# Kernel optimization log

Measured on AMD Instinct MI355X. Metric: run time of the kernel, lower is better.

Reference implementation:

```python
import jax, jax.numpy as jnp
import numpy as np

NEG_SLOPE = 0.01  # torch nn.LeakyReLU default
N_NODES, N_EDGES, N_BATCH, L_PATH = 100000, 300000, 50000, 4
D_EMB, D_HID, N_HEADS = 128, 64, 8


def setup_inputs() -> dict:
    key = jax.random.key(0)
    ks = jax.random.split(key, 10)
    return {
        "batch_nodes": jax.random.randint(ks[0], (N_BATCH,), 0, N_NODES),
        "metapath_indices": jax.random.randint(ks[1], (N_EDGES, L_PATH), 0, N_NODES),
        "edge_dst": jax.random.randint(ks[2], (N_EDGES,), 0, N_NODES),
        "transformed_feature": jax.random.normal(ks[3], (N_NODES, D_EMB), jnp.float32),
        "W_i": jax.random.normal(ks[4], (D_HID, D_EMB), jnp.float32) * 0.05,
        "W_p": jax.random.normal(ks[5], (D_HID, D_EMB), jnp.float32) * 0.05,
        "attn": jax.random.normal(ks[6], (1, N_HEADS, D_HID), jnp.float32) * 0.05,
        "W_th": jax.random.normal(ks[7], (N_HEADS, N_HEADS), jnp.float32) * 0.3,
        "W_gate": jax.random.normal(ks[8], (1, D_HID), jnp.float32) * 0.1,
        "b_gate": jnp.zeros((1,), jnp.float32),
    }


def reference(batch_nodes, metapath_indices, edge_dst, transformed_feature,
              W_i, W_p, attn, W_th, W_gate, b_gate):
    N = transformed_feature.shape[0]
    # node_type_specific_agg for mtype==1: h_src/h_dst through linear_i, h_p1/h_p2 through linear_p
    membd = transformed_feature[metapath_indices]                      # [E, 4, D_emb]
    edata = (membd[:, 0] + membd[:, 3]) @ W_i.T \
          + (membd[:, 1] + membd[:, 2]) @ W_p.T                        # [E, D]
    E, D = edata.shape
    H = attn.shape[1]
    # cat([edata]*H, dim=1).view(-1, H, D) duplicates edata per head
    efeat = jnp.broadcast_to(edata[:, None, :], (E, H, D))             # [E, H, D]
    # talking-heads attention logits, leaky-relu
    logits = (efeat * attn).sum(-1) @ W_th.T                           # [E, H]
    logits = jax.nn.leaky_relu(logits, NEG_SLOPE)
    # dgl edge_softmax: per-dst-node, per-head softmax over incoming edges (stable)
    m = jax.ops.segment_max(logits, edge_dst, num_segments=N)          # [N, H]
    ex = jnp.exp(logits - m[edge_dst])                                 # [E, H]
    den = jax.ops.segment_sum(ex, edge_dst, num_segments=N)            # [N, H]
    a = ex / den[edge_dst]                                             # [E, H]  (dropout rate 0)
    # message passing: ft = efeature * a, summed per dst node
    msgs = (efeat * a[:, :, None]).reshape(E, H * D)
    node_ft = jax.ops.segment_sum(msgs, edge_dst, num_segments=N)      # [N, H*D]
    result = node_ft[batch_nodes].reshape(-1, H, D)                    # [B, H, D]
    # gated multi-head attention: gate = mean over batch of fc_gate(result)
    gate = jnp.mean(result @ W_gate.T + b_gate, axis=0)                # [H, 1]
    result = result * gate[None]                                       # [B, H, D]
    return result.reshape(-1, H * D)
```

## Files before the change

### kernel.cpp

```cpp
#include <hip/hip_runtime.h>
#include <cstdint>
#include <cstddef>


typedef __attribute__((ext_vector_type(8))) short bf16x8;
typedef __attribute__((ext_vector_type(4))) float f32x4;
typedef __attribute__((ext_vector_type(8))) unsigned short u16x8;

__device__ __forceinline__ unsigned short f2bf(float f) {
    unsigned u = __float_as_uint(f);
    unsigned r = u + 0x7fffu + ((u >> 16) & 1u);
    return (unsigned short)(r >> 16);
}
__device__ __forceinline__ float bf2f(unsigned short h) {
    return __uint_as_float((unsigned)h << 16);
}
__device__ __forceinline__ unsigned fenc(float f) {
    unsigned u = __float_as_uint(f);
    return (u & 0x80000000u) ? ~u : (u | 0x80000000u);
}
__device__ __forceinline__ float fdec(unsigned k) {
    unsigned u = (k & 0x80000000u) ? (k & 0x7fffffffu) : ~k;
    return __uint_as_float(u);
}

__global__ __launch_bounds__(256) void k_prep(
    const float* __restrict__ Wi, const float* __restrict__ Wp,
    const float* __restrict__ attn,
    unsigned short* __restrict__ Whi, unsigned short* __restrict__ Wlo,
    unsigned short* __restrict__ Phi, unsigned short* __restrict__ Plo,
    const int* __restrict__ batch_nodes, int* __restrict__ mult, int B) {
    int t = blockIdx.x * 256 + threadIdx.x;
    if (t < B) atomicAdd(&mult[batch_nodes[t]], 1);
    if (t < 16384) {
        int j = t & 7, L = (t >> 3) & 63, c = (t >> 9) & 7, s = t >> 12;
        int k = s * 32 + (L >> 4) * 8 + j;
        int n = c * 16 + (L & 15);
        float v = (n < 64) ? Wi[n * 128 + k] : Wp[(n - 64) * 128 + k];
        unsigned short h = f2bf(v);
        Whi[t] = h;
        Wlo[t] = f2bf(v - bf2f(h));
    } else if (t < 16384 + 2048) {
        int t2 = t - 16384;
        int j = t2 & 7, L = (t2 >> 3) & 63, s = t2 >> 9;
        int k = s * 32 + (L >> 4) * 8 + j;
        int i = L & 15;
        const float* Wsrc = (i < 8) ? Wi : Wp;
        const float* av = attn + (size_t)(i & 7) * 64;
        float v = 0.f;
#pragma unroll 8
        for (int d = 0; d < 64; ++d) v += av[d] * Wsrc[d * 128 + k];
        unsigned short h = f2bf(v);
        Phi[t2] = h;
        Plo[t2] = f2bf(v - bf2f(h));
    }
}

__global__ __launch_bounds__(256, 4) void k_dense(
    const float* __restrict__ feat, const unsigned short* __restrict__ Whi,
    const unsigned short* __restrict__ Wlo, const unsigned short* __restrict__ Phi,
    const unsigned short* __restrict__ Plo,
    const int* __restrict__ edge_dst, const int* __restrict__ mult,
    int* __restrict__ count, unsigned short* __restrict__ Ybf,
    float* __restrict__ P, int M, int E) {
    int t = threadIdx.x;

    {
        int e = blockIdx.x * 256 + t;
        if (e < E) {
            int d = edge_dst[e];
            if (mult[d] > 0) atomicAdd(&count[d], 1);
        }
    }

    int L = t & 63;
    int wave = t >> 6;
    int m = L & 15, q = L >> 4;
    int R0 = blockIdx.x * 64 + wave * 16;

    int rowc = R0 + m; if (rowc > M - 1) rowc = M - 1;
    const float* arow = feat + (size_t)rowc * 128;

    float4 av0[4], av1[4];
#pragma unroll
    for (int s = 0; s < 4; ++s) {
        const float4* ap = (const float4*)(arow + s * 32 + q * 8);
        av0[s] = ap[0];
        av1[s] = ap[1];
    }
    bf16x8 ahi[4], alo[4];
#pragma unroll
    for (int s = 0; s < 4; ++s) {
        float av[8] = {av0[s].x, av0[s].y, av0[s].z, av0[s].w,
                       av1[s].x, av1[s].y, av1[s].z, av1[s].w};
#pragma unroll
        for (int j = 0; j < 8; ++j) {
            unsigned short h = f2bf(av[j]);
            ahi[s][j] = (short)h;
            alo[s][j] = (short)f2bf(av[j] - bf2f(h));
        }
    }

    f32x4 acc[8];
#pragma unroll
    for (int c = 0; c < 8; ++c) acc[c] = (f32x4){0.f, 0.f, 0.f, 0.f};
    f32x4 accP = (f32x4){0.f, 0.f, 0.f, 0.f};

    const bf16x8* gh = (const bf16x8*)Whi;
    const bf16x8* gl = (const bf16x8*)Wlo;
    const bf16x8* ph = (const bf16x8*)Phi;
    const bf16x8* pl = (const bf16x8*)Plo;
#pragma unroll
    for (int s = 0; s < 4; ++s) {
#pragma unroll
        for (int c = 0; c < 8; ++c) {
            bf16x8 bh = gh[(s * 8 + c) * 64 + L];
            bf16x8 bl = gl[(s * 8 + c) * 64 + L];
            acc[c] = __builtin_amdgcn_mfma_f32_16x16x32_bf16(ahi[s], bh, acc[c], 0, 0, 0);
            acc[c] = __builtin_amdgcn_mfma_f32_16x16x32_bf16(ahi[s], bl, acc[c], 0, 0, 0);
            acc[c] = __builtin_amdgcn_mfma_f32_16x16x32_bf16(alo[s], bh, acc[c], 0, 0, 0);
        }
        {
            bf16x8 bh = ph[s * 64 + L];
            bf16x8 bl = pl[s * 64 + L];
            accP = __builtin_amdgcn_mfma_f32_16x16x32_bf16(ahi[s], bh, accP, 0, 0, 0);
            accP = __builtin_amdgcn_mfma_f32_16x16x32_bf16(ahi[s], bl, accP, 0, 0, 0);
            accP = __builtin_amdgcn_mfma_f32_16x16x32_bf16(alo[s], bh, accP, 0, 0, 0);
        }
    }

#pragma unroll
    for (int c = 0; c < 8; ++c) {
#pragma unroll
        for (int r = 0; r < 4; ++r) {
            int row = R0 + q * 4 + r;
            if (row < M) Ybf[(size_t)row * 128 + c * 16 + m] = f2bf(acc[c][r]);
        }
    }
#pragma unroll
    for (int r = 0; r < 4; ++r) {
        int row = R0 + q * 4 + r;
        if (row < M) P[(size_t)row * 16 + m] = accP[r];
    }
}

__global__ __launch_bounds__(256) void k_scan1(
    const int* __restrict__ count, int* __restrict__ excl, int* __restrict__ partials, int N) {
    __shared__ int lds[256];
    int t = threadIdx.x, i = blockIdx.x * 256 + t;
    int c = (i < N) ? count[i] : 0;
    lds[t] = c; __syncthreads();
    for (int o = 1; o < 256; o <<= 1) {
        int v = (t >= o) ? lds[t - o] : 0;
        __syncthreads(); lds[t] += v; __syncthreads();
    }
    if (i < N) excl[i] = lds[t] - c;
    if (t == 255) partials[blockIdx.x] = lds[255];
}

__global__ __launch_bounds__(256) void k_scan23(
    const int* __restrict__ excl, const int* __restrict__ partials,
    int* __restrict__ offsets, int* __restrict__ cursor, int N) {
    __shared__ int sacc[256];
    int bid = blockIdx.x, t = threadIdx.x;
    int s = 0;
    for (int j = t; j < bid; j += 256) s += partials[j];
    sacc[t] = s; __syncthreads();
#pragma unroll
    for (int o = 128; o > 0; o >>= 1) {
        if (t < o) sacc[t] += sacc[t + o];
        __syncthreads();
    }
    int boff = sacc[0];
    int i = bid * 256 + t;
    if (i < N) {
        int o = excl[i] + boff;
        offsets[i] = o; cursor[i] = o;
    }
    if (t == 0 && bid == gridDim.x - 1) offsets[N] = boff + partials[bid];
}

__global__ __launch_bounds__(256) void k_scatter_logits(
    const int* __restrict__ edge_dst, const int* __restrict__ mult,
    int* __restrict__ cursor, const int* __restrict__ mp,
    const float* __restrict__ P, const float* __restrict__ Wth,
    float* __restrict__ logits, int4* __restrict__ mpc,
    unsigned* __restrict__ mxkey, int E) {
    int e = blockIdx.x * 32 + (threadIdx.x >> 3);
    if (e >= E) return;
    int h = threadIdx.x & 7;
    int d = edge_dst[e];
    if (mult[d] == 0) return;
    int pos = 0;
    if (h == 0) pos = atomicAdd(&cursor[d], 1);
    int gbase = threadIdx.x & ~7;
    pos = __shfl(pos, gbase);
    int4 rows = *(const int4*)(mp + (size_t)e * 4);
    float s = P[(size_t)rows.x * 16 + h] + P[(size_t)rows.w * 16 + h]
            + P[(size_t)rows.y * 16 + 8 + h] + P[(size_t)rows.z * 16 + 8 + h];
    float l = 0.f;
#pragma unroll
    for (int j = 0; j < 8; ++j) {
        float sj = __shfl(s, gbase + j);
        l += Wth[h * 8 + j] * sj;
    }
    l = l > 0.f ? l : 0.01f * l;
    logits[(size_t)pos * 8 + h] = l;
    atomicMax(&mxkey[(size_t)d * 8 + h], fenc(l));
    if (h == 0) mpc[pos] = rows;
}

__global__ __launch_bounds__(256) void k_node_agg(
    const unsigned short* __restrict__ Ybf, const float* __restrict__ logits,
    const int4* __restrict__ mpc, const int* __restrict__ offsets,
    const int* __restrict__ mult, const unsigned* __restrict__ mxkey,
    const float* __restrict__ Wg,
    unsigned short* __restrict__ nftb, float* __restrict__ gate_part, int N) {
    int lane = threadIdx.x & 63;
    int gwave = blockIdx.x * 4 + (threadIdx.x >> 6);
    int nwaves = gridDim.x * 4;
    float wg = Wg[lane];

    float gp[8];
#pragma unroll
    for (int h = 0; h < 8; ++h) gp[h] = 0.f;

    for (int n = gwave; n < N; n += nwaves) {
        int m = mult[n];
        if (m == 0) continue;
        int beg = offsets[n], end = offsets[n + 1];

        float mx[8], den[8], acc[8];
#pragma unroll
        for (int h = 0; h < 8; ++h) {
            mx[h] = fdec(mxkey[(size_t)n * 8 + h]);
            den[h] = 0.f; acc[h] = 0.f;
        }

        for (int j = beg; j < end; ++j) {
            const float4* lp = (const float4*)(logits + (size_t)j * 8);
            float4 l0 = lp[0], l1 = lp[1];
            int4 rows = mpc[j];
            float ed = bf2f(Ybf[(size_t)rows.x * 128 + lane])
                     + bf2f(Ybf[(size_t)rows.w * 128 + lane])
                     + bf2f(Ybf[(size_t)rows.y * 128 + 64 + lane])
                     + bf2f(Ybf[(size_t)rows.z * 128 + 64 + lane]);
            float w0 = __expf(l0.x - mx[0]), w1 = __expf(l0.y - mx[1]);
            float w2 = __expf(l0.z - mx[2]), w3 = __expf(l0.w - mx[3]);
            float w4 = __expf(l1.x - mx[4]), w5 = __expf(l1.y - mx[5]);
            float w6 = __expf(l1.z - mx[6]), w7 = __expf(l1.w - mx[7]);
            den[0] += w0; den[1] += w1; den[2] += w2; den[3] += w3;
            den[4] += w4; den[5] += w5; den[6] += w6; den[7] += w7;
            acc[0] += w0 * ed; acc[1] += w1 * ed; acc[2] += w2 * ed; acc[3] += w3 * ed;
            acc[4] += w4 * ed; acc[5] += w5 * ed; acc[6] += w6 * ed; acc[7] += w7 * ed;
        }

#pragma unroll
        for (int h = 0; h < 8; ++h) {
            float r = (end > beg) ? 1.f / den[h] : 0.f;
            acc[h] *= r;
        }

        unsigned short* base = nftb + (size_t)n * 512;
#pragma unroll
        for (int h = 0; h < 8; ++h) base[h * 64 + lane] = f2bf(acc[h]);

#pragma unroll
        for (int h = 0; h < 8; ++h) gp[h] += (float)m * acc[h];
    }

    float myg = 0.f;
#pragma unroll
    for (int h = 0; h < 8; ++h) {
        float p = gp[h] * wg;
#pragma unroll
        for (int o = 32; o > 0; o >>= 1) p += __shfl_xor(p, o);
        if (lane == h) myg = p;
    }
    if (lane < 8)
        atomicAdd(&gate_part[(blockIdx.x & 255) * 8 + lane], myg);
}

__global__ __launch_bounds__(256) void k_output(
    const unsigned short* __restrict__ nftb, const int* __restrict__ batch_nodes,
    const float* __restrict__ gate_part, const float* __restrict__ b_gate,
    float* __restrict__ out, int B) {
    __shared__ float lds[256];
    __shared__ float sg[8];
    int t = threadIdx.x;
    {
        int h = t & 7, g = t >> 3;
        float s = 0.f;
        for (int b = g; b < 256; b += 32) s += gate_part[b * 8 + h];
        lds[t] = s; __syncthreads();
        if (t < 8) {
            float tot = 0.f;
            for (int gg = 0; gg < 32; ++gg) tot += lds[gg * 8 + t];
            sg[t] = tot / (float)B + b_gate[0];
        }
        __syncthreads();
    }
    int idx = blockIdx.x * 256 + t;
    int total = B * 64;
    if (idx >= total) return;
    int b = idx >> 6;
    int r = idx & 63;
    int h = r >> 3;
    int n = batch_nodes[b];
    u16x8 v = *(const u16x8*)(nftb + (size_t)n * 512 + r * 8);
    float g = sg[h];
    f32x4 o0, o1;
    o0[0] = bf2f(v[0]) * g; o0[1] = bf2f(v[1]) * g;
    o0[2] = bf2f(v[2]) * g; o0[3] = bf2f(v[3]) * g;
    o1[0] = bf2f(v[4]) * g; o1[1] = bf2f(v[5]) * g;
    o1[2] = bf2f(v[6]) * g; o1[3] = bf2f(v[7]) * g;
    f32x4* op = (f32x4*)(out + (size_t)idx * 8);
    __builtin_nontemporal_store(o0, op);
    __builtin_nontemporal_store(o1, op + 1);
}

extern "C" void kernel_launch(void* const* d_in, const int* in_sizes, int n_in,
                              void* d_out, int out_size, void* d_ws, size_t ws_size,
                              hipStream_t stream) {
    const int*   batch_nodes = (const int*)d_in[0];
    const int*   mp          = (const int*)d_in[1];
    const int*   edge_dst    = (const int*)d_in[2];
    const float* feat        = (const float*)d_in[3];
    const float* W_i         = (const float*)d_in[4];
    const float* W_p         = (const float*)d_in[5];
    const float* attn        = (const float*)d_in[6];
    const float* W_th        = (const float*)d_in[7];
    const float* W_gate      = (const float*)d_in[8];
    const float* b_gate      = (const float*)d_in[9];
    float* out = (float*)d_out;

    const int B = in_sizes[0];
    const int E = in_sizes[2];
    const int N = in_sizes[3] / 128;
    const int nb_scan = (N + 255) / 256;

    char* w = (char*)d_ws;
    auto alloc = [&](size_t bytes) -> void* {
        void* p = (void*)w;
        w += (bytes + 255) & ~(size_t)255;
        return p;
    };
    unsigned short* Whi = (unsigned short*)alloc(16384 * 2);
    unsigned short* Wlo = (unsigned short*)alloc(16384 * 2);
    unsigned short* Phi = (unsigned short*)alloc(2048 * 2);
    unsigned short* Plo = (unsigned short*)alloc(2048 * 2);
    unsigned short* Ybf = (unsigned short*)alloc((size_t)N * 128 * 2);
    float* P            = (float*)alloc((size_t)N * 16 * 4);
    float* logits       = (float*)alloc((size_t)E * 8 * 4);
    int4*  mpc          = (int4*)alloc((size_t)E * 16);
    size_t zero_bytes   = (size_t)N * 4 + (size_t)N * 4 + 256 * 8 * 4
                        + (size_t)N * 8 * 4;
    int*   mult         = (int*)alloc(zero_bytes);
    int*   count        = mult + N;
    float* gate_part    = (float*)(count + N);
    unsigned* mxkey     = (unsigned*)(gate_part + 256 * 8);
    int*   excl         = (int*)alloc((size_t)N * 4);
    int*   offsets      = (int*)alloc((size_t)(N + 1) * 4);
    int*   cursor       = (int*)alloc((size_t)N * 4);
    int*   partials     = (int*)alloc(512 * 4);
    unsigned short* nftb = (unsigned short*)alloc((size_t)N * 512 * 2);

    hipMemsetAsync(mult, 0, zero_bytes, stream);

    int prep_work = (B > 16384 + 2048) ? B : 16384 + 2048;
    k_prep<<<(prep_work + 255) / 256, 256, 0, stream>>>(W_i, W_p, attn,
                                                        Whi, Wlo, Phi, Plo,
                                                        batch_nodes, mult, B);
    k_dense<<<(N + 63) / 64, 256, 0, stream>>>(feat, Whi, Wlo, Phi, Plo,
                                               edge_dst, mult, count, Ybf, P, N, E);
    k_scan1<<<nb_scan, 256, 0, stream>>>(count, excl, partials, N);
    k_scan23<<<nb_scan, 256, 0, stream>>>(excl, partials, offsets, cursor, N);
    k_scatter_logits<<<(E + 31) / 32, 256, 0, stream>>>(edge_dst, mult, cursor,
                                                        mp, P, W_th, logits, mpc,
                                                        mxkey, E);
    k_node_agg<<<2048, 256, 0, stream>>>(Ybf, logits, mpc, offsets, mult,
                                         mxkey, W_gate, nftb, gate_part, N);
    k_output<<<(B * 64 + 255) / 256, 256, 0, stream>>>(nftb, batch_nodes,
                                                       gate_part, b_gate, out, B);
}
```

Baseline: 303.4 us.

## Precompute per-edge bf16 edata in scatter kernel instead of gathering in aggregation

The scatter kernel now runs one wavefront per edge, gathers the four Ybf rows, sums them into the 64-wide edge feature, and writes it as bf16 into CSR-sorted order. The aggregation kernel then reads that edge feature contiguously instead of doing four random row gathers per edge, and the int4 row-index buffer is dropped. This moves the random gathers earlier, into a kernel that is highly parallel, and makes the serial per-node loop stream contiguous data. The cost is an extra E*128-byte write and read, a scatter launch with eight times more threads, and an extra bf16 rounding of the summed edge feature.

```diff
diff --git a/kernel.cpp b/kernel.cpp
--- a/kernel.cpp
+++ b/kernel.cpp
@@ -183,38 +183,43 @@
 __global__ __launch_bounds__(256) void k_scatter_logits(
     const int* __restrict__ edge_dst, const int* __restrict__ mult,
     int* __restrict__ cursor, const int* __restrict__ mp,
-    const float* __restrict__ P, const float* __restrict__ Wth,
-    float* __restrict__ logits, int4* __restrict__ mpc,
-    unsigned* __restrict__ mxkey, int E) {
-    int e = blockIdx.x * 32 + (threadIdx.x >> 3);
+    const unsigned short* __restrict__ Ybf, const float* __restrict__ P,
+    const float* __restrict__ Wth, float* __restrict__ logits,
+    unsigned short* __restrict__ edata, unsigned* __restrict__ mxkey, int E) {
+    int e = blockIdx.x * 4 + (threadIdx.x >> 6);
+    int lane = threadIdx.x & 63;
     if (e >= E) return;
-    int h = threadIdx.x & 7;
     int d = edge_dst[e];
     if (mult[d] == 0) return;
+    int4 rows = *(const int4*)(mp + (size_t)e * 4);
+    float ed = bf2f(Ybf[(size_t)rows.x * 128 + lane])
+             + bf2f(Ybf[(size_t)rows.w * 128 + lane])
+             + bf2f(Ybf[(size_t)rows.y * 128 + 64 + lane])
+             + bf2f(Ybf[(size_t)rows.z * 128 + 64 + lane]);
     int pos = 0;
-    if (h == 0) pos = atomicAdd(&cursor[d], 1);
-    int gbase = threadIdx.x & ~7;
-    pos = __shfl(pos, gbase);
-    int4 rows = *(const int4*)(mp + (size_t)e * 4);
-    float s = P[(size_t)rows.x * 16 + h] + P[(size_t)rows.w * 16 + h]
-            + P[(size_t)rows.y * 16 + 8 + h] + P[(size_t)rows.z * 16 + 8 + h];
-    float l = 0.f;
-#pragma unroll
-    for (int j = 0; j < 8; ++j) {
-        float sj = __shfl(s, gbase + j);
-        l += Wth[h * 8 + j] * sj;
-    }
-    l = l > 0.f ? l : 0.01f * l;
-    logits[(size_t)pos * 8 + h] = l;
-    atomicMax(&mxkey[(size_t)d * 8 + h], fenc(l));
-    if (h == 0) mpc[pos] = rows;
+    if (lane == 0) pos = atomicAdd(&cursor[d], 1);
+    pos = __shfl(pos, 0);
+    edata[(size_t)pos * 64 + lane] = f2bf(ed);
+    if (lane < 8) {
+        int h = lane;
+        float s = P[(size_t)rows.x * 16 + h] + P[(size_t)rows.w * 16 + h]
+                + P[(size_t)rows.y * 16 + 8 + h] + P[(size_t)rows.z * 16 + 8 + h];
+        float l = 0.f;
+#pragma unroll
+        for (int j = 0; j < 8; ++j) {
+            float sj = __shfl(s, j);
+            l += Wth[h * 8 + j] * sj;
+        }
+        l = l > 0.f ? l : 0.01f * l;
+        logits[(size_t)pos * 8 + h] = l;
+        atomicMax(&mxkey[(size_t)d * 8 + h], fenc(l));
+    }
 }
 
 __global__ __launch_bounds__(256) void k_node_agg(
-    const unsigned short* __restrict__ Ybf, const float* __restrict__ logits,
-    const int4* __restrict__ mpc, const int* __restrict__ offsets,
-    const int* __restrict__ mult, const unsigned* __restrict__ mxkey,
-    const float* __restrict__ Wg,
+    const float* __restrict__ logits, const unsigned short* __restrict__ edata,
+    const int* __restrict__ offsets, const int* __restrict__ mult,
+    const unsigned* __restrict__ mxkey, const float* __restrict__ Wg,
     unsigned short* __restrict__ nftb, float* __restrict__ gate_part, int N) {
     int lane = threadIdx.x & 63;
     int gwave = blockIdx.x * 4 + (threadIdx.x >> 6);
@@ -240,11 +245,7 @@
         for (int j = beg; j < end; ++j) {
             const float4* lp = (const float4*)(logits + (size_t)j * 8);
             float4 l0 = lp[0], l1 = lp[1];
-            int4 rows = mpc[j];
-            float ed = bf2f(Ybf[(size_t)rows.x * 128 + lane])
-                     + bf2f(Ybf[(size_t)rows.w * 128 + lane])
-                     + bf2f(Ybf[(size_t)rows.y * 128 + 64 + lane])
-                     + bf2f(Ybf[(size_t)rows.z * 128 + 64 + lane]);
+            float ed = bf2f(edata[(size_t)j * 64 + lane]);
             float w0 = __expf(l0.x - mx[0]), w1 = __expf(l0.y - mx[1]);
             float w2 = __expf(l0.z - mx[2]), w3 = __expf(l0.w - mx[3]);
             float w4 = __expf(l1.x - mx[4]), w5 = __expf(l1.y - mx[5]);
@@ -352,7 +353,7 @@
     unsigned short* Ybf = (unsigned short*)alloc((size_t)N * 128 * 2);
     float* P            = (float*)alloc((size_t)N * 16 * 4);
     float* logits       = (float*)alloc((size_t)E * 8 * 4);
-    int4*  mpc          = (int4*)alloc((size_t)E * 16);
+    unsigned short* edata = (unsigned short*)alloc((size_t)E * 64 * 2);
     size_t zero_bytes   = (size_t)N * 4 + (size_t)N * 4 + 256 * 8 * 4
                         + (size_t)N * 8 * 4;
     int*   mult         = (int*)alloc(zero_bytes);
@@ -375,10 +376,10 @@
                                                edge_dst, mult, count, Ybf, P, N, E);
     k_scan1<<<nb_scan, 256, 0, stream>>>(count, excl, partials, N);
     k_scan23<<<nb_scan, 256, 0, stream>>>(excl, partials, offsets, cursor, N);
-    k_scatter_logits<<<(E + 31) / 32, 256, 0, stream>>>(edge_dst, mult, cursor,
-                                                        mp, P, W_th, logits, mpc,
-                                                        mxkey, E);
-    k_node_agg<<<2048, 256, 0, stream>>>(Ybf, logits, mpc, offsets, mult,
+    k_scatter_logits<<<(E + 3) / 4, 256, 0, stream>>>(edge_dst, mult, cursor,
+                                                      mp, Ybf, P, W_th, logits,
+                                                      edata, mxkey, E);
+    k_node_agg<<<2048, 256, 0, stream>>>(logits, edata, offsets, mult,
                                          mxkey, W_gate, nftb, gate_part, N);
     k_output<<<(B * 64 + 255) / 256, 256, 0, stream>>>(nftb, batch_nodes,
                                                        gate_part, b_gate, out, B);
```

Result: slower. 342.1 us (+12.8%).
